# Performance work log

Hardware: AMD Instinct MI355X
Metric: run time of the kernel (lower is better)

Reference implementation:

```python
import jax, jax.numpy as jnp
import numpy as np

D_MODEL = 1024
STATE = 16

def setup_inputs() -> dict:
    key = jax.random.key(0)
    ks = jax.random.split(key, 7)
    x = jax.random.normal(ks[0], (4, 4096, D_MODEL), dtype=jnp.float32)
    A_log = jax.random.normal(ks[1], (STATE,), dtype=jnp.float32)
    B = jax.random.normal(ks[2], (STATE, D_MODEL), dtype=jnp.float32) * 0.05
    C = jax.random.normal(ks[3], (D_MODEL, STATE), dtype=jnp.float32) * 0.05
    D = jax.random.normal(ks[4], (D_MODEL,), dtype=jnp.float32)
    W_delta = jax.random.normal(ks[5], (D_MODEL, D_MODEL), dtype=jnp.float32) * 0.02
    b_delta = jax.random.normal(ks[6], (D_MODEL,), dtype=jnp.float32) * 0.02
    return {"x": x, "A_log": A_log, "B": B, "C": C, "D": D,
            "W_delta": W_delta, "b_delta": b_delta}

def reference(x, A_log, B, C, D, W_delta, b_delta):
    # delta: softplus(Linear(x)).mean(-1) -> (b, l)
    delta = jax.nn.softplus(jnp.einsum('bld,ed->ble', x, W_delta) + b_delta).mean(-1)
    A = -jnp.exp(A_log)                         # (n,)
    Bx = jnp.einsum('bld,nd->bln', x, B)        # (b, l, n)
    dA = jnp.exp(delta[..., None] * A)          # (b, l, n)
    dBx = delta[..., None] * Bx                 # (b, l, n)

    def step(h, inp):
        dA_t, dBx_t = inp                       # (b, n) each
        h = dA_t * h + dBx_t
        return h, h

    h0 = jnp.zeros((x.shape[0], A_log.shape[0]), dtype=x.dtype)
    _, hs = jax.lax.scan(step, h0, (jnp.swapaxes(dA, 0, 1), jnp.swapaxes(dBx, 0, 1)))
    hs = jnp.swapaxes(hs, 0, 1)                 # (b, l, n)
    y = jnp.einsum('bln,dn->bld', hs, C) + D * x
    return y
```

## Files before the change

kernel.cpp:

```cpp
#include <hip/hip_runtime.h>
#include <hip/hip_bf16.h>
#include <stdint.h>

#define DM 1024
#define NS 16
#define LSEQ 4096
#define NB 4
#define MTOT (NB*LSEQ)
#define NC 128
#define LC 32

typedef __attribute__((ext_vector_type(8))) short bf16x8;
typedef __attribute__((ext_vector_type(4))) float f32x4;

__device__ __forceinline__ unsigned short f2bf(float f) {
    unsigned int u = __float_as_uint(f);
    unsigned int r = (u + 0x7FFFu + ((u >> 16) & 1u)) >> 16;
    return (unsigned short)r;
}

__device__ __forceinline__ float bf2f(unsigned short u) {
    return __uint_as_float(((unsigned int)u) << 16);
}

__device__ __forceinline__ float softplus_f(float v) {
    return v > 15.f ? v : __logf(1.f + __expf(v));
}

__device__ __forceinline__ void gload_lds16(const void* g, void* l) {
    __builtin_amdgcn_global_load_lds(
        (const __attribute__((address_space(1))) unsigned int*)g,
        (__attribute__((address_space(3))) unsigned int*)l, 16, 0, 0);
}

__global__ __launch_bounds__(256) void pre_kernel(
    const float4* __restrict__ x4, const float4* __restrict__ W4,
    const float4* __restrict__ B4, ushort4* __restrict__ xb4,
    ushort4* __restrict__ wb4, ushort4* __restrict__ bbf4,
    float* __restrict__ delta_raw)
{
    int bid = blockIdx.x, t = threadIdx.x;
    if (bid < 16384) {
        size_t i = (size_t)bid * 256 + t;
        float4 v = x4[i];
        ushort4 o; o.x = f2bf(v.x); o.y = f2bf(v.y); o.z = f2bf(v.z); o.w = f2bf(v.w);
        xb4[i] = o;
    } else if (bid < 17408) {
        int i = (bid - 16384) * 256 + t;
        float4 v = W4[i];
        ushort4 o; o.x = f2bf(v.x); o.y = f2bf(v.y); o.z = f2bf(v.z); o.w = f2bf(v.w);
        wb4[i] = o;
    } else if (bid < 17424) {
        int i = (bid - 17408) * 256 + t;
        float4 v = B4[i];
        ushort4 o; o.x = f2bf(v.x); o.y = f2bf(v.y); o.z = f2bf(v.z); o.w = f2bf(v.w);
        bbf4[i] = o;
    } else {
        int i = (bid - 17424) * 256 + t;
        ((float4*)delta_raw)[i] = (float4){0.f, 0.f, 0.f, 0.f};
    }
}

__global__ __launch_bounds__(512) void gemm_delta(
    const unsigned short* __restrict__ xb, const unsigned short* __restrict__ wb,
    const float* __restrict__ b_delta, float* __restrict__ delta_raw)
{
    __shared__ char lds[131072];
    int bid = blockIdx.x;
    int swz = (bid & 7) * 32 + (bid >> 3);
    int mb = swz >> 2, nb = swz & 3;
    int row0 = mb * 256, e0 = nb * 256;
    int tid = threadIdx.x;
    int lane = tid & 63, w = tid >> 6;
    int wr = w >> 2, wc = w & 3;
    int lm = lane & 15, lk = lane >> 4;

    int colsw = ((lane & 7) * 8) ^ ((lane >> 3) << 3);
    int rsub = lane >> 3;

    const unsigned short* pA[4];
    const unsigned short* pB[4];
    #pragma unroll
    for (int j = 0; j < 4; ++j) {
        int region = w * 4 + j;
        int r0 = region * 8 + rsub;
        pA[j] = xb + (size_t)(row0 + r0) * DM + colsw;
        pB[j] = wb + (size_t)(e0  + r0) * DM + colsw;
    }

    int sterm = (lm & 7) << 4;
    int off0 = (lk * 16) ^ sterm;
    int off1 = (64 + lk * 16) ^ sterm;
    int aBase = (wr * 128 + lm) * 128;
    int bBase = 32768 + (wc * 64 + lm) * 128;

    f32x4 acc[8][4];
    #pragma unroll
    for (int m = 0; m < 8; ++m)
        #pragma unroll
        for (int n = 0; n < 4; ++n)
            acc[m][n] = (f32x4){0.f, 0.f, 0.f, 0.f};

    bf16x8 bq[4][2];

#define STAGE_Q(BUF, Q, KOFF) do { \
    gload_lds16(pA[Q] + (KOFF), lds + (BUF) + ((w * 4 + (Q)) * 1024)); \
    gload_lds16(pB[Q] + (KOFF), lds + (BUF) + 32768 + ((w * 4 + (Q)) * 1024)); \
} while (0)

#define PHASE(CUR, NXT, KOFF, STG, Q) do { \
    if (STG) STAGE_Q(NXT, Q, KOFF); \
    if ((Q) == 0) { \
        if (STG) asm volatile("s_waitcnt vmcnt(2)\n\ts_barrier" ::: "memory"); \
        else     asm volatile("s_waitcnt vmcnt(0)\n\ts_barrier" ::: "memory"); \
        _Pragma("unroll") \
        for (int n = 0; n < 4; ++n) { \
            bq[n][0] = *(const bf16x8*)(lds + (CUR) + bBase + n * 2048 + off0); \
            bq[n][1] = *(const bf16x8*)(lds + (CUR) + bBase + n * 2048 + off1); \
        } \
    } \
    bf16x8 a0 = *(const bf16x8*)(lds + (CUR) + aBase + (2*(Q)) * 2048 + off0); \
    bf16x8 a1 = *(const bf16x8*)(lds + (CUR) + aBase + (2*(Q)) * 2048 + off1); \
    bf16x8 a2 = *(const bf16x8*)(lds + (CUR) + aBase + (2*(Q)+1) * 2048 + off0); \
    bf16x8 a3 = *(const bf16x8*)(lds + (CUR) + aBase + (2*(Q)+1) * 2048 + off1); \
    asm volatile("s_barrier" ::: "memory"); \
    __builtin_amdgcn_s_setprio(1); \
    _Pragma("unroll") \
    for (int n = 0; n < 4; ++n) { \
        acc[2*(Q)][n]   = __builtin_amdgcn_mfma_f32_16x16x32_bf16(a0, bq[n][0], acc[2*(Q)][n], 0, 0, 0); \
        acc[2*(Q)][n]   = __builtin_amdgcn_mfma_f32_16x16x32_bf16(a1, bq[n][1], acc[2*(Q)][n], 0, 0, 0); \
        acc[2*(Q)+1][n] = __builtin_amdgcn_mfma_f32_16x16x32_bf16(a2, bq[n][0], acc[2*(Q)+1][n], 0, 0, 0); \
        acc[2*(Q)+1][n] = __builtin_amdgcn_mfma_f32_16x16x32_bf16(a3, bq[n][1], acc[2*(Q)+1][n], 0, 0, 0); \
    } \
    __builtin_amdgcn_s_setprio(0); \
    asm volatile("s_barrier" ::: "memory"); \
} while (0)

#define KTILE(CUR, NXT, KOFF, STG) do { \
    PHASE(CUR, NXT, KOFF, STG, 0); \
    PHASE(CUR, NXT, KOFF, STG, 1); \
    PHASE(CUR, NXT, KOFF, STG, 2); \
    PHASE(CUR, NXT, KOFF, STG, 3); \
} while (0)

    STAGE_Q(0, 0, 0); STAGE_Q(0, 1, 0); STAGE_Q(0, 2, 0); STAGE_Q(0, 3, 0);
    int koff = 64;
    #pragma unroll 1
    for (int it = 0; it < 7; ++it) {
        KTILE(0,     65536, koff,      true);
        KTILE(65536, 0,     koff + 64, true);
        koff += 128;
    }
    KTILE(0, 65536, 960, true);
    KTILE(65536, 0, 0, false);

#undef KTILE
#undef PHASE
#undef STAGE_Q

    float bd[4];
    #pragma unroll
    for (int n = 0; n < 4; ++n) bd[n] = b_delta[e0 + wc * 64 + n * 16 + lm];
    #pragma unroll
    for (int m = 0; m < 8; ++m) {
        #pragma unroll
        for (int r = 0; r < 4; ++r) {
            float s = 0.f;
            #pragma unroll
            for (int n = 0; n < 4; ++n) s += softplus_f(acc[m][n][r] + bd[n]);
            s += __shfl_xor(s, 1, 16);
            s += __shfl_xor(s, 2, 16);
            s += __shfl_xor(s, 4, 16);
            s += __shfl_xor(s, 8, 16);
            if (lm == 0) {
                int row = row0 + wr * 128 + m * 16 + lk * 4 + r;
                atomicAdd(&delta_raw[row], s);
            }
        }
    }
}

__global__ __launch_bounds__(256) void bx_mfma(
    const unsigned short* __restrict__ xb, const unsigned short* __restrict__ bbf,
    float* __restrict__ Bx)
{
    int tid = threadIdx.x, lane = tid & 63, w = tid >> 6;
    int rb = blockIdx.x * 4 + w;
    int r0 = rb * 16;
    int lm = lane & 15, lk = lane >> 4;
    const unsigned short* pa = xb + (size_t)(r0 + lm) * DM + lk * 8;
    const unsigned short* pb = bbf + (size_t)lm * DM + lk * 8;
    f32x4 acc = (f32x4){0.f, 0.f, 0.f, 0.f};
    #pragma unroll 4
    for (int k0 = 0; k0 < DM; k0 += 32) {
        bf16x8 a = *(const bf16x8*)(pa + k0);
        bf16x8 b = *(const bf16x8*)(pb + k0);
        acc = __builtin_amdgcn_mfma_f32_16x16x32_bf16(a, b, acc, 0, 0, 0);
    }
    #pragma unroll
    for (int r = 0; r < 4; ++r)
        Bx[(size_t)(r0 + lk * 4 + r) * NS + lm] = acc[r];
}

__global__ __launch_bounds__(64) void scan_pass1(
    const float* __restrict__ delta_raw, const float* __restrict__ Bx,
    const float* __restrict__ A_log, float* __restrict__ cP, float* __restrict__ cH)
{
    __shared__ float dl[LC];
    __shared__ float bxl[LC * NS];
    int bid = blockIdx.x;
    int b = bid >> 7, c = bid & 127;
    int l0 = c * LC;
    int t = threadIdx.x;
    size_t base = (size_t)b * LSEQ + l0;
    if (t < LC) dl[t] = delta_raw[base + t] * (1.f / 1024.f);
    const float4* src = (const float4*)(Bx + base * NS);
    float4* dst = (float4*)bxl;
    dst[t] = src[t];
    dst[t + 64] = src[t + 64];
    __syncthreads();
    if (t < NS) {
        float a = -__expf(A_log[t]);
        float P = 1.f, h = 0.f;
        #pragma unroll
        for (int s = 0; s < LC; ++s) {
            float dlt = dl[s];
            float dA = __expf(dlt * a);
            h = dA * h + dlt * bxl[s * NS + t];
            P *= dA;
        }
        int idx = (b * NC + c) * NS + t;
        cP[idx] = P; cH[idx] = h;
    }
}

__global__ __launch_bounds__(256) void y_kernel(
    const unsigned short* __restrict__ xb, const float* __restrict__ delta_raw,
    const float* __restrict__ Bx, const float* __restrict__ A_log,
    const float* __restrict__ cP, const float* __restrict__ cH,
    const float* __restrict__ C, const float* __restrict__ Dv, float* __restrict__ y)
{
    __shared__ float dl[LC];
    __shared__ float bxl[LC * NS];
    __shared__ float hsl[LC * NS];
    __shared__ float pbuf[NC * NS];
    __shared__ float hbuf[NC * NS];
    int bid = blockIdx.x;
    int b = bid >> 7, c = bid & 127;
    int l0 = c * LC;
    int t = threadIdx.x;
    size_t base = (size_t)b * LSEQ + l0;
    if (t < LC) dl[t] = delta_raw[base + t] * (1.f / 1024.f);
    if (t < 128) ((float4*)bxl)[t] = ((const float4*)(Bx + base * NS))[t];
    {
        const float4* p4 = (const float4*)(cP + (size_t)b * NC * NS);
        const float4* h4 = (const float4*)(cH + (size_t)b * NC * NS);
        ((float4*)pbuf)[t] = p4[t];         ((float4*)pbuf)[t + 256] = p4[t + 256];
        ((float4*)hbuf)[t] = h4[t];         ((float4*)hbuf)[t + 256] = h4[t + 256];
    }
    __syncthreads();
    if (t < NS) {
        float h = 0.f;
        for (int cc = 0; cc < c; ++cc) {
            int idx = cc * NS + t;
            h = pbuf[idx] * h + hbuf[idx];
        }
        float a = -__expf(A_log[t]);
        #pragma unroll
        for (int s = 0; s < LC; ++s) {
            float dlt = dl[s];
            float dA = __expf(dlt * a);
            h = dA * h + dlt * bxl[s * NS + t];
            hsl[s * NS + t] = h;
        }
    }
    __syncthreads();

    int d0 = t * 4;
    float cr[4][NS];
    #pragma unroll
    for (int dd = 0; dd < 4; ++dd)
        #pragma unroll
        for (int nn = 0; nn < 4; ++nn) {
            float4 c4 = ((const float4*)C)[((d0 + dd) * NS + nn * 4) >> 2];
            cr[dd][nn * 4 + 0] = c4.x; cr[dd][nn * 4 + 1] = c4.y;
            cr[dd][nn * 4 + 2] = c4.z; cr[dd][nn * 4 + 3] = c4.w;
        }
    float4 dv = ((const float4*)Dv)[t];
    const ushort4* xr = (const ushort4*)(xb + base * DM) + t;
    float4* yr = (float4*)(y + base * DM) + t;
    for (int s = 0; s < LC; ++s) {
        float hv[NS];
        #pragma unroll
        for (int n = 0; n < NS; ++n) hv[n] = hsl[s * NS + n];
        ushort4 xv4 = xr[s * 256];
        float4 o;
        o.x = dv.x * bf2f(xv4.x); o.y = dv.y * bf2f(xv4.y);
        o.z = dv.z * bf2f(xv4.z); o.w = dv.w * bf2f(xv4.w);
        #pragma unroll
        for (int n = 0; n < NS; ++n) {
            o.x += hv[n] * cr[0][n];
            o.y += hv[n] * cr[1][n];
            o.z += hv[n] * cr[2][n];
            o.w += hv[n] * cr[3][n];
        }
        yr[s * 256] = o;
    }
}

extern "C" void kernel_launch(void* const* d_in, const int* in_sizes, int n_in,
                              void* d_out, int out_size, void* d_ws, size_t ws_size,
                              hipStream_t stream)
{
    const float* x     = (const float*)d_in[0];
    const float* A_log = (const float*)d_in[1];
    const float* B     = (const float*)d_in[2];
    const float* C     = (const float*)d_in[3];
    const float* Dv    = (const float*)d_in[4];
    const float* Wd    = (const float*)d_in[5];
    const float* bd    = (const float*)d_in[6];
    float* y = (float*)d_out;

    char* ws = (char*)d_ws;
    unsigned short* xb = (unsigned short*)ws;
    unsigned short* wb = (unsigned short*)(ws + 33554432);
    float* delta_raw   = (float*)(ws + 35651584);
    float* Bx          = (float*)(ws + 35717120);
    float* cP          = (float*)(ws + 36765696);
    float* cH          = (float*)(ws + 36798464);
    unsigned short* bbf= (unsigned short*)(ws + 36831232);

    pre_kernel<<<17440, 256, 0, stream>>>((const float4*)x, (const float4*)Wd,
                                          (const float4*)B, (ushort4*)xb,
                                          (ushort4*)wb, (ushort4*)bbf, delta_raw);
    gemm_delta<<<256, 512, 0, stream>>>(xb, wb, bd, delta_raw);
    bx_mfma<<<256, 256, 0, stream>>>(xb, bbf, Bx);
    scan_pass1<<<NB * NC, 64, 0, stream>>>(delta_raw, Bx, A_log, cP, cH);
    y_kernel<<<NB * NC, 256, 0, stream>>>(xb, delta_raw, Bx, A_log, cP, cH, C, Dv, y);
}
```

Baseline: 94.09 us.

## Fuse Bx projection into delta GEMM reusing staged x tiles

Removes the separate bx_mfma kernel. The first column-block (nb==0) of each row tile in gemm_delta now also computes the B·x projection, reusing the A fragments already loaded from LDS and reading the small B matrix directly from global memory. This drops one kernel launch and a second full read of xb. In exchange, a quarter of the blocks carry extra MFMAs and global loads inside the pipelined loop, which can create imbalance and add register pressure.

```diff
diff --git a/kernel.cpp b/kernel.cpp
--- a/kernel.cpp
+++ b/kernel.cpp
@@ -63,7 +63,8 @@
 
 __global__ __launch_bounds__(512) void gemm_delta(
     const unsigned short* __restrict__ xb, const unsigned short* __restrict__ wb,
-    const float* __restrict__ b_delta, float* __restrict__ delta_raw)
+    const unsigned short* __restrict__ bbf, const float* __restrict__ b_delta,
+    float* __restrict__ delta_raw, float* __restrict__ Bx)
 {
     __shared__ char lds[131072];
     int bid = blockIdx.x;
@@ -74,6 +75,7 @@
     int lane = tid & 63, w = tid >> 6;
     int wr = w >> 2, wc = w & 3;
     int lm = lane & 15, lk = lane >> 4;
+    bool doBx = (nb == 0);
 
     int colsw = ((lane & 7) * 8) ^ ((lane >> 3) << 3);
     int rsub = lane >> 3;
@@ -87,6 +89,7 @@
         pA[j] = xb + (size_t)(row0 + r0) * DM + colsw;
         pB[j] = wb + (size_t)(e0  + r0) * DM + colsw;
     }
+    const unsigned short* pBB = bbf + (size_t)lm * DM + lk * 8;
 
     int sterm = (lm & 7) << 4;
     int off0 = (lk * 16) ^ sterm;
@@ -100,19 +103,26 @@
         #pragma unroll
         for (int n = 0; n < 4; ++n)
             acc[m][n] = (f32x4){0.f, 0.f, 0.f, 0.f};
+    f32x4 bxacc0 = (f32x4){0.f, 0.f, 0.f, 0.f};
+    f32x4 bxacc1 = (f32x4){0.f, 0.f, 0.f, 0.f};
 
     bf16x8 bq[4][2];
+    bf16x8 bb0, bb1;
 
 #define STAGE_Q(BUF, Q, KOFF) do { \
     gload_lds16(pA[Q] + (KOFF), lds + (BUF) + ((w * 4 + (Q)) * 1024)); \
     gload_lds16(pB[Q] + (KOFF), lds + (BUF) + 32768 + ((w * 4 + (Q)) * 1024)); \
 } while (0)
 
-#define PHASE(CUR, NXT, KOFF, STG, Q) do { \
+#define PHASE(CUR, NXT, KOFF, KBB, STG, Q) do { \
     if (STG) STAGE_Q(NXT, Q, KOFF); \
     if ((Q) == 0) { \
         if (STG) asm volatile("s_waitcnt vmcnt(2)\n\ts_barrier" ::: "memory"); \
         else     asm volatile("s_waitcnt vmcnt(0)\n\ts_barrier" ::: "memory"); \
+        if (doBx) { \
+            bb0 = *(const bf16x8*)(pBB + (KBB)); \
+            bb1 = *(const bf16x8*)(pBB + (KBB) + 32); \
+        } \
         _Pragma("unroll") \
         for (int n = 0; n < 4; ++n) { \
             bq[n][0] = *(const bf16x8*)(lds + (CUR) + bBase + n * 2048 + off0); \
@@ -132,31 +142,46 @@
         acc[2*(Q)+1][n] = __builtin_amdgcn_mfma_f32_16x16x32_bf16(a2, bq[n][0], acc[2*(Q)+1][n], 0, 0, 0); \
         acc[2*(Q)+1][n] = __builtin_amdgcn_mfma_f32_16x16x32_bf16(a3, bq[n][1], acc[2*(Q)+1][n], 0, 0, 0); \
     } \
+    if (doBx && wc == (Q)) { \
+        bxacc0 = __builtin_amdgcn_mfma_f32_16x16x32_bf16(a0, bb0, bxacc0, 0, 0, 0); \
+        bxacc0 = __builtin_amdgcn_mfma_f32_16x16x32_bf16(a1, bb1, bxacc0, 0, 0, 0); \
+        bxacc1 = __builtin_amdgcn_mfma_f32_16x16x32_bf16(a2, bb0, bxacc1, 0, 0, 0); \
+        bxacc1 = __builtin_amdgcn_mfma_f32_16x16x32_bf16(a3, bb1, bxacc1, 0, 0, 0); \
+    } \
     __builtin_amdgcn_s_setprio(0); \
     asm volatile("s_barrier" ::: "memory"); \
 } while (0)
 
-#define KTILE(CUR, NXT, KOFF, STG) do { \
-    PHASE(CUR, NXT, KOFF, STG, 0); \
-    PHASE(CUR, NXT, KOFF, STG, 1); \
-    PHASE(CUR, NXT, KOFF, STG, 2); \
-    PHASE(CUR, NXT, KOFF, STG, 3); \
+#define KTILE(CUR, NXT, KOFF, KBB, STG) do { \
+    PHASE(CUR, NXT, KOFF, KBB, STG, 0); \
+    PHASE(CUR, NXT, KOFF, KBB, STG, 1); \
+    PHASE(CUR, NXT, KOFF, KBB, STG, 2); \
+    PHASE(CUR, NXT, KOFF, KBB, STG, 3); \
 } while (0)
 
     STAGE_Q(0, 0, 0); STAGE_Q(0, 1, 0); STAGE_Q(0, 2, 0); STAGE_Q(0, 3, 0);
     int koff = 64;
     #pragma unroll 1
     for (int it = 0; it < 7; ++it) {
-        KTILE(0,     65536, koff,      true);
-        KTILE(65536, 0,     koff + 64, true);
+        KTILE(0,     65536, koff,      koff - 64, true);
+        KTILE(65536, 0,     koff + 64, koff,      true);
         koff += 128;
     }
-    KTILE(0, 65536, 960, true);
-    KTILE(65536, 0, 0, false);
+    KTILE(0, 65536, 960, 896, true);
+    KTILE(65536, 0, 0, 960, false);
 
 #undef KTILE
 #undef PHASE
 #undef STAGE_Q
+
+    if (doBx) {
+        #pragma unroll
+        for (int r = 0; r < 4; ++r) {
+            int row = row0 + wr * 128 + wc * 32 + lk * 4 + r;
+            Bx[(size_t)row * NS + lm] = bxacc0[r];
+            Bx[(size_t)(row + 16) * NS + lm] = bxacc1[r];
+        }
+    }
 
     float bd[4];
     #pragma unroll
@@ -178,28 +203,6 @@
             }
         }
     }
-}
-
-__global__ __launch_bounds__(256) void bx_mfma(
-    const unsigned short* __restrict__ xb, const unsigned short* __restrict__ bbf,
-    float* __restrict__ Bx)
-{
-    int tid = threadIdx.x, lane = tid & 63, w = tid >> 6;
-    int rb = blockIdx.x * 4 + w;
-    int r0 = rb * 16;
-    int lm = lane & 15, lk = lane >> 4;
-    const unsigned short* pa = xb + (size_t)(r0 + lm) * DM + lk * 8;
-    const unsigned short* pb = bbf + (size_t)lm * DM + lk * 8;
-    f32x4 acc = (f32x4){0.f, 0.f, 0.f, 0.f};
-    #pragma unroll 4
-    for (int k0 = 0; k0 < DM; k0 += 32) {
-        bf16x8 a = *(const bf16x8*)(pa + k0);
-        bf16x8 b = *(const bf16x8*)(pb + k0);
-        acc = __builtin_amdgcn_mfma_f32_16x16x32_bf16(a, b, acc, 0, 0, 0);
-    }
-    #pragma unroll
-    for (int r = 0; r < 4; ++r)
-        Bx[(size_t)(r0 + lk * 4 + r) * NS + lm] = acc[r];
 }
 
 __global__ __launch_bounds__(64) void scan_pass1(
@@ -333,8 +336,7 @@
     pre_kernel<<<17440, 256, 0, stream>>>((const float4*)x, (const float4*)Wd,
                                           (const float4*)B, (ushort4*)xb,
                                           (ushort4*)wb, (ushort4*)bbf, delta_raw);
-    gemm_delta<<<256, 512, 0, stream>>>(xb, wb, bd, delta_raw);
-    bx_mfma<<<256, 256, 0, stream>>>(xb, bbf, Bx);
+    gemm_delta<<<256, 512, 0, stream>>>(xb, wb, bbf, bd, delta_raw, Bx);
     scan_pass1<<<NB * NC, 64, 0, stream>>>(delta_raw, Bx, A_log, cP, cH);
     y_kernel<<<NB * NC, 256, 0, stream>>>(xb, delta_raw, Bx, A_log, cP, cH, C, Dv, y);
 }
```

Result: slower. 97.18 us (+3.3%).
